# Optimization experiments

Measured on AMD Instinct MI355X. Metric: run time of the kernel, lower is better.

The kernel has to match this reference:

```python
import jax, jax.numpy as jnp
import numpy as np

COORD_DIM = 2
NUM_CHANNELS = 3
LATENT = 128
HIDDEN = 64
N0 = 8192
RADIUS = 0.035
RADII = (RADIUS, 2.0 * RADIUS)
ITER_COUNT = 3


def _radius_edges(y, x, r):
    # y: (Ny,d) source points, x: (Nx,d) query points -> edge lists (src into y, dst into x)
    d2 = ((x[:, None, :] - y[None, :, :]) ** 2).sum(-1)
    dst, src = np.nonzero(d2 <= r * r)
    return jnp.asarray(src, jnp.int32), jnp.asarray(dst, jnp.int32)


def setup_inputs():
    rng = np.random.default_rng(0)
    coords_np = rng.uniform(size=(COORD_DIM, N0)).astype(np.float32)
    c0 = coords_np.T            # (N0, d) fine level
    c1 = coords_np[:, ::2].T    # (N1, d) coarse level (stride-2 subsample)
    r_cross = max(RADII)
    e01_src, e01_dst = _radius_edges(c0, c1, r_cross)   # GK_0_1: y=lvl0, x=lvl1
    e10_src, e10_dst = _radius_edges(c1, c0, r_cross)   # GK_1_0: y=lvl1, x=lvl0
    e00_src, e00_dst = _radius_edges(c0, c0, RADII[0])  # GK_0_0
    e11_src, e11_dst = _radius_edges(c1, c1, RADII[1])  # GK_1_1

    key = jax.random.key(0)
    ks = iter(jax.random.split(key, 40))

    def lin(fi, fo):
        return jax.random.normal(next(ks), (fi, fo), jnp.float32) / np.float32(np.sqrt(fi))

    inp = dict(
        coords=jnp.asarray(coords_np),
        samples=jax.random.normal(next(ks), (N0, NUM_CHANNELS), jnp.float32),
        sigma=jax.random.uniform(next(ks), (1,), jnp.float32),
        fc_lift_w=lin(NUM_CHANNELS, LATENT), fc_lift_b=jnp.zeros((LATENT,), jnp.float32),
        fc_proj_w=lin(LATENT, NUM_CHANNELS), fc_proj_b=jnp.zeros((NUM_CHANNELS,), jnp.float32),
        W0_w=lin(LATENT, LATENT), W0_b=jnp.zeros((LATENT,), jnp.float32),
        W1_w=lin(LATENT, LATENT), W1_b=jnp.zeros((LATENT,), jnp.float32),
    )
    for name in ("gk00", "gk01", "gk10", "gk11"):
        inp[name + "_w1"] = lin(2 * COORD_DIM, HIDDEN)
        inp[name + "_b1"] = jnp.zeros((HIDDEN,), jnp.float32)
        inp[name + "_w2"] = lin(HIDDEN, LATENT)
        inp[name + "_b2"] = jnp.zeros((LATENT,), jnp.float32)
    inp.update(e00_src=e00_src, e00_dst=e00_dst, e01_src=e01_src, e01_dst=e01_dst,
               e10_src=e10_src, e10_dst=e10_dst, e11_src=e11_src, e11_dst=e11_dst)
    return inp


def _gno(xc, yc, f_y, src, dst, w1, b1, w2, b2, num_x):
    # gather -> edge kernel MLP on concat coords -> modulate by f_y -> scatter-mean
    e = jnp.concatenate([yc[src], xc[dst]], axis=1)        # (E, 2d)
    k = jax.nn.gelu(e @ w1 + b1) @ w2 + b2                 # (E, C) kernel values
    msg = k * f_y[src]                                     # 'linear' integral transform
    out = jax.ops.segment_sum(msg, dst, num_segments=num_x)
    cnt = jax.ops.segment_sum(jnp.ones(src.shape, msg.dtype), dst, num_segments=num_x)
    return out / jnp.maximum(cnt, 1.0)[:, None]


def reference(coords, samples, sigma,
              fc_lift_w, fc_lift_b, fc_proj_w, fc_proj_b,
              W0_w, W0_b, W1_w, W1_b,
              gk00_w1, gk00_b1, gk00_w2, gk00_b2,
              gk01_w1, gk01_b1, gk01_w2, gk01_b2,
              gk10_w1, gk10_b1, gk10_w2, gk10_b2,
              gk11_w1, gk11_b1, gk11_w2, gk11_b2,
              e00_src, e00_dst, e01_src, e01_dst,
              e10_src, e10_dst, e11_src, e11_dst):
    c0 = coords.T            # (N0, d)
    c1 = coords[:, ::2].T    # (N1, d)
    n0, n1 = c0.shape[0], c1.shape[0]
    v_down0 = samples @ fc_lift_w + fc_lift_b   # lifted features, never overwritten at level 0
    v_up0 = v_down0
    v_up1 = None
    for _ in range(ITER_COUNT):
        # downward pass (l = 1)
        vd = _gno(c1, c0, v_down0, e01_src, e01_dst, gk01_w1, gk01_b1, gk01_w2, gk01_b2, n1)
        if v_up1 is not None:
            vd = vd + v_up1
        v_down1 = jax.nn.relu(vd)
        # bottom level update
        v_up1 = jax.nn.relu(v_down1 @ W1_w + W1_b
                            + _gno(c1, c1, v_down1, e11_src, e11_dst, gk11_w1, gk11_b1, gk11_w2, gk11_b2, n1))
        # upward pass (l = 0)
        vu = _gno(c0, c1, v_up1, e10_src, e10_dst, gk10_w1, gk10_b1, gk10_w2, gk10_b2, n0)
        vu = vu + v_down0 @ W0_w + W0_b \
             + _gno(c0, c0, v_down0, e00_src, e00_dst, gk00_w1, gk00_b1, gk00_w2, gk00_b2, n0)
        v_up0 = jax.nn.relu(vu)
    return v_up0 @ fc_proj_w + fc_proj_b   # (N0, num_channels)
```

## Files before the change

### kernel.cpp

```cpp
#include <hip/hip_runtime.h>
#include <hip/hip_bf16.h>

typedef __attribute__((ext_vector_type(8))) short s8;
typedef __attribute__((ext_vector_type(4))) float f4;

__device__ __forceinline__ float gelu_fast(float x) {
    float x2 = x * x;
    float k  = x * fmaf(x2, 0.07135481624f, 1.59576912161f);
    float e  = __expf(k);
    float r  = __builtin_amdgcn_rcpf(e + 1.f);
    return x - x * r;
}

__device__ __forceinline__ short f2bf_bits(float v) {
    __hip_bfloat16 b = __float2bfloat16(v);
    return *(short*)&b;
}

struct RP { const int* edst; int E; int N; int* rowptr; };

__global__ void rowptr4_kernel(RP a, RP b, RP c, RP d) {
    RP g = (blockIdx.y == 0) ? a : (blockIdx.y == 1) ? b : (blockIdx.y == 2) ? c : d;
    int i = blockIdx.x * blockDim.x + threadIdx.x;
    if (i >= g.E) return;
    int dd = g.edst[i];
    int p  = (i == 0) ? -1 : g.edst[i - 1];
    for (int r = p + 1; r <= dd; ++r) g.rowptr[r] = i;
    if (i == g.E - 1)
        for (int r = dd + 1; r <= g.N; ++r) g.rowptr[r] = g.E;
}

__global__ __launch_bounds__(128) void pack_w2_kernel(
    const float* __restrict__ wa, const float* __restrict__ wb,
    const float* __restrict__ wc, const float* __restrict__ wd,
    short* __restrict__ out)
{
    const float* w2 = (blockIdx.x == 0) ? wa : (blockIdx.x == 1) ? wb
                    : (blockIdx.x == 2) ? wc : wd;
    short* dst = out + (size_t)blockIdx.x * 8192;
    const int t = threadIdx.x;
    const int w = t >> 6, lane = t & 63, q = (lane >> 4), n = lane & 15;
#pragma unroll
    for (int T = 0; T < 4; ++T)
#pragma unroll
        for (int s = 0; s < 2; ++s)
#pragma unroll
            for (int j = 0; j < 8; ++j) {
                int k  = s * 32 + q * 8 + j;
                int ch = 64 * w + 16 * T + n;
                dst[((((w * 4 + T) * 2 + s) * 64) + lane) * 8 + j] =
                    f2bf_bits(w2[k * 128 + ch]);
            }
}

__global__ __launch_bounds__(128) void gno_kernel(
    const float* __restrict__ coords, int n0, int sx, int sy,
    const float* __restrict__ f_y,
    const int* __restrict__ esrc, const int* __restrict__ rowptr,
    const float* __restrict__ w1, const float* __restrict__ b1,
    const short* __restrict__ w2bf, const float* __restrict__ b2,
    const float* __restrict__ add0, const float* __restrict__ add1,
    int do_relu, float* __restrict__ out,
    const float* __restrict__ projw, const float* __restrict__ projb,
    float* __restrict__ fout)
{
    const int b = blockIdx.x, t = threadIdx.x;
    const int w = t >> 6, lane = t & 63, q = lane >> 4, n = lane & 15;
    const int h = lane;

    __shared__ int   s_src[16];
    __shared__ float s_yx[16], s_yy[16];
    __shared__ __align__(16) short s_gb[16 * 72];
    __shared__ float sred[6];

    const float rw0 = w1[h], rw1 = w1[64 + h];
    const float xcx = coords[(long)b * sx];
    const float xcy = coords[n0 + (long)b * sx];
    const float xcc = xcx * w1[128 + h] + xcy * w1[192 + h] + b1[h];

    s8 bfrag[4][2];
    const s8* w2f = (const s8*)w2bf;
#pragma unroll
    for (int T = 0; T < 4; ++T)
#pragma unroll
        for (int s = 0; s < 2; ++s)
            bfrag[T][s] = w2f[((w * 4 + T) * 2 + s) * 64 + lane];

    float b2c[4];
#pragma unroll
    for (int T = 0; T < 4; ++T) b2c[T] = b2[w * 64 + T * 16 + n];

    const int lo = rowptr[b], hi = rowptr[b + 1];

    float acc4[4] = {0.f, 0.f, 0.f, 0.f};

    for (int base = lo; base < hi; base += 16) {
        const int cnt = min(16, hi - base);
        if (t < 16) {
            int e = base + t; if (e >= hi) e = hi - 1;
            int sv = esrc[e];
            s_src[t] = sv;
            s_yx[t]  = coords[(long)sv * sy];
            s_yy[t]  = coords[n0 + (long)sv * sy];
        }
        __syncthreads();
        float fv[4][4];
#pragma unroll
        for (int r = 0; r < 4; ++r) {
            int m = q * 4 + r;
            bool valid = m < cnt;
            long srow = (long)s_src[m] * 128;
#pragma unroll
            for (int T = 0; T < 4; ++T)
                fv[r][T] = valid ? f_y[srow + w * 64 + T * 16 + n] : 0.f;
        }
#pragma unroll
        for (int i = 0; i < 8; ++i) {
            int j = 2 * i + w;
            float x = fmaf(s_yx[j], rw0, fmaf(s_yy[j], rw1, xcc));
            s_gb[j * 72 + h] = f2bf_bits(gelu_fast(x));
        }
        __syncthreads();
        const s8 a0 = *(const s8*)&s_gb[n * 72 + q * 8];
        const s8 a1 = *(const s8*)&s_gb[n * 72 + q * 8 + 32];
        f4 c[4];
#pragma unroll
        for (int T = 0; T < 4; ++T) {
            f4 z = {0.f, 0.f, 0.f, 0.f};
            z = __builtin_amdgcn_mfma_f32_16x16x32_bf16(a0, bfrag[T][0], z, 0, 0, 0);
            c[T] = __builtin_amdgcn_mfma_f32_16x16x32_bf16(a1, bfrag[T][1], z, 0, 0, 0);
        }
#pragma unroll
        for (int r = 0; r < 4; ++r)
#pragma unroll
            for (int T = 0; T < 4; ++T)
                acc4[T] += (c[T][r] + b2c[T]) * fv[r][T];
    }

    const float inv = 1.f / fmaxf((float)(hi - lo), 1.f);
    float res4[4];
#pragma unroll
    for (int T = 0; T < 4; ++T) {
        float v = acc4[T];
        v += __shfl_xor(v, 16, 64);
        v += __shfl_xor(v, 32, 64);
        long o = (long)b * 128 + w * 64 + T * 16 + n;
        float res = v * inv;
        if (add0) res += add0[o];
        if (add1) res += add1[o];
        if (do_relu) res = fmaxf(res, 0.f);
        res4[T] = res;
    }
    if (!projw) {
        if (q == 0)
#pragma unroll
            for (int T = 0; T < 4; ++T)
                out[(long)b * 128 + w * 64 + T * 16 + n] = res4[T];
    } else {
        __syncthreads();
        float* s_pr = (float*)s_gb;
        if (q == 0)
#pragma unroll
            for (int T = 0; T < 4; ++T) s_pr[w * 64 + T * 16 + n] = res4[T];
        __syncthreads();
        float v = s_pr[t];
        float p0 = v * projw[t * 3 + 0];
        float p1 = v * projw[t * 3 + 1];
        float p2 = v * projw[t * 3 + 2];
#pragma unroll
        for (int o = 32; o > 0; o >>= 1) {
            p0 += __shfl_down(p0, o);
            p1 += __shfl_down(p1, o);
            p2 += __shfl_down(p2, o);
        }
        if (lane == 0) { sred[w * 3 + 0] = p0; sred[w * 3 + 1] = p1; sred[w * 3 + 2] = p2; }
        __syncthreads();
        if (t < 3) fout[b * 3 + t] = sred[t] + sred[3 + t] + projb[t];
    }
}

__global__ __launch_bounds__(128) void fused_relu_mm_kernel(
    const float* __restrict__ base, const float* __restrict__ addl,
    float* __restrict__ vout,
    const float* __restrict__ W, const float* __restrict__ bias,
    float* __restrict__ out, int R)
{
    const int r0 = blockIdx.x * 8;
    const int t = threadIdx.x;
    __shared__ float s_x[8 * 128];
#pragma unroll
    for (int j = 0; j < 8; ++j) {
        int r = r0 + j;
        if (r < R) {
            long o = (long)r * 128 + t;
            float v = base[o] + (addl ? addl[o] : 0.f);
            v = fmaxf(v, 0.f);
            s_x[j * 128 + t] = v;
            vout[o] = v;
        } else s_x[j * 128 + t] = 0.f;
    }
    __syncthreads();
    float acc[8];
    const float bc = bias[t];
#pragma unroll
    for (int j = 0; j < 8; ++j) acc[j] = bc;
    for (int hh = 0; hh < 128; ++hh) {
        float wv = W[hh * 128 + t];
#pragma unroll
        for (int j = 0; j < 8; ++j) acc[j] += s_x[j * 128 + hh] * wv;
    }
#pragma unroll
    for (int j = 0; j < 8; ++j) {
        int r = r0 + j;
        if (r < R) out[(long)r * 128 + t] = acc[j];
    }
}

__global__ __launch_bounds__(128) void matmul128_kernel(
    const float* __restrict__ X, const float* __restrict__ W,
    const float* __restrict__ bias, float* __restrict__ out, int R)
{
    const int r0 = blockIdx.x * 8;
    const int t = threadIdx.x;
    __shared__ float s_x[8 * 128];
#pragma unroll
    for (int j = 0; j < 8; ++j) {
        int r = r0 + j;
        s_x[j * 128 + t] = (r < R) ? X[(long)r * 128 + t] : 0.f;
    }
    __syncthreads();
    float acc[8];
    const float bc = bias[t];
#pragma unroll
    for (int j = 0; j < 8; ++j) acc[j] = bc;
    for (int hh = 0; hh < 128; ++hh) {
        float wv = W[hh * 128 + t];
#pragma unroll
        for (int j = 0; j < 8; ++j) acc[j] += s_x[j * 128 + hh] * wv;
    }
#pragma unroll
    for (int j = 0; j < 8; ++j) {
        int r = r0 + j;
        if (r < R) out[(long)r * 128 + t] = acc[j];
    }
}

__global__ __launch_bounds__(128) void lift_kernel(
    const float* __restrict__ samples, const float* __restrict__ W,
    const float* __restrict__ bias, float* __restrict__ out, int N)
{
    const int i = blockIdx.x;
    const int t = threadIdx.x;
    float s0 = samples[i * 3 + 0];
    float s1 = samples[i * 3 + 1];
    float s2 = samples[i * 3 + 2];
    out[(long)i * 128 + t] = s0 * W[t] + s1 * W[128 + t] + s2 * W[256 + t] + bias[t];
}

extern "C" void kernel_launch(void* const* d_in, const int* in_sizes, int n_in,
                              void* d_out, int out_size, void* d_ws, size_t ws_size,
                              hipStream_t stream)
{
    const float* coords  = (const float*)d_in[0];
    const float* samples = (const float*)d_in[1];
    const float* lift_w  = (const float*)d_in[3];
    const float* lift_b  = (const float*)d_in[4];
    const float* proj_w  = (const float*)d_in[5];
    const float* proj_b  = (const float*)d_in[6];
    const float* W0_w    = (const float*)d_in[7];
    const float* W0_b    = (const float*)d_in[8];
    const float* W1_w    = (const float*)d_in[9];
    const float* W1_b    = (const float*)d_in[10];
    const float *gw1[4], *gb1[4], *gw2[4], *gb2[4];
    for (int g = 0; g < 4; ++g) {
        gw1[g] = (const float*)d_in[11 + 4 * g + 0];
        gb1[g] = (const float*)d_in[11 + 4 * g + 1];
        gw2[g] = (const float*)d_in[11 + 4 * g + 2];
        gb2[g] = (const float*)d_in[11 + 4 * g + 3];
    }
    const int* es[4]; const int* ed[4]; int E[4];
    for (int g = 0; g < 4; ++g) {
        es[g] = (const int*)d_in[27 + 2 * g];
        ed[g] = (const int*)d_in[27 + 2 * g + 1];
        E[g]  = in_sizes[27 + 2 * g];
    }

    const int N0 = in_sizes[0] / 2;
    const int N1 = (N0 + 1) / 2;

    float* ws = (float*)d_ws;
    float* v_down0 = ws;
    float* w0term  = v_down0 + (size_t)N0 * 128;
    float* gno00o  = w0term  + (size_t)N0 * 128;
    float* gno01b  = gno00o  + (size_t)N0 * 128;
    float* v_down1 = gno01b  + (size_t)N1 * 128;
    float* w1term  = v_down1 + (size_t)N1 * 128;
    float* v_up1   = w1term  + (size_t)N1 * 128;
    short* w2pack  = (short*)(v_up1 + (size_t)N1 * 128);
    int*   rp      = (int*)(w2pack + 4 * 8192);
    int* rp00 = rp;
    int* rp01 = rp00 + (N0 + 1);
    int* rp10 = rp01 + (N1 + 1);
    int* rp11 = rp10 + (N0 + 1);
    int* rptr[4] = {rp00, rp01, rp10, rp11};
    int  rpN[4]  = {N0, N1, N0, N1};

    {
        int maxE = E[0];
        for (int g = 1; g < 4; ++g) maxE = max(maxE, E[g]);
        RP a = {ed[0], E[0], rpN[0], rptr[0]};
        RP b = {ed[1], E[1], rpN[1], rptr[1]};
        RP c = {ed[2], E[2], rpN[2], rptr[2]};
        RP d = {ed[3], E[3], rpN[3], rptr[3]};
        dim3 grid((maxE + 255) / 256, 4);
        rowptr4_kernel<<<grid, 256, 0, stream>>>(a, b, c, d);
    }
    pack_w2_kernel<<<4, 128, 0, stream>>>(gw2[0], gw2[1], gw2[2], gw2[3], w2pack);

    lift_kernel<<<N0, 128, 0, stream>>>(samples, lift_w, lift_b, v_down0, N0);
    matmul128_kernel<<<(N0 + 7) / 8, 128, 0, stream>>>(v_down0, W0_w, W0_b, w0term, N0);
    gno_kernel<<<N0, 128, 0, stream>>>(coords, N0, 1, 1, v_down0,
        es[0], rp00, gw1[0], gb1[0], w2pack + 0 * 8192, gb2[0],
        nullptr, nullptr, 0, gno00o, nullptr, nullptr, nullptr);
    gno_kernel<<<N1, 128, 0, stream>>>(coords, N0, 2, 1, v_down0,
        es[1], rp01, gw1[1], gb1[1], w2pack + 1 * 8192, gb2[1],
        nullptr, nullptr, 0, gno01b, nullptr, nullptr, nullptr);

    for (int it = 0; it < 3; ++it) {
        fused_relu_mm_kernel<<<(N1 + 7) / 8, 128, 0, stream>>>(
            gno01b, (it == 0) ? nullptr : v_up1, v_down1, W1_w, W1_b, w1term, N1);
        gno_kernel<<<N1, 128, 0, stream>>>(coords, N0, 2, 2, v_down1,
            es[3], rp11, gw1[3], gb1[3], w2pack + 3 * 8192, gb2[3],
            w1term, nullptr, 1, v_up1, nullptr, nullptr, nullptr);
    }

    gno_kernel<<<N0, 128, 0, stream>>>(coords, N0, 1, 2, v_up1,
        es[2], rp10, gw1[2], gb1[2], w2pack + 2 * 8192, gb2[2],
        w0term, gno00o, 1, nullptr, proj_w, proj_b, (float*)d_out);
}
```

Measured before the change: 368.5 us.

## Process multiple destination nodes per GNO block with double-buffered edge staging

Each GNO block now handles a chunk of consecutive destination nodes (4 at fine level, 2 at coarse) so it can reuse the loaded W2 fragments and layer-1 weights. Edge source indices and coordinates are prefetched 64 at a time into double-buffered shared memory, and the GELU tile buffer is also double-buffered so one barrier per 16-edge group can be dropped. W2 is repacked so each lane owns four contiguous output channels, which turns feature gathers, bias and output stores into float4 accesses. The grid shrinks, so there are fewer blocks to hide latency, and the loop control becomes more complex.

```diff
diff --git a/kernel.cpp b/kernel.cpp
--- a/kernel.cpp
+++ b/kernel.cpp
@@ -47,7 +47,7 @@
 #pragma unroll
             for (int j = 0; j < 8; ++j) {
                 int k  = s * 32 + q * 8 + j;
-                int ch = 64 * w + 16 * T + n;
+                int ch = 64 * w + 4 * n + T;
                 dst[((((w * 4 + T) * 2 + s) * 64) + lane) * 8 + j] =
                     f2bf_bits(w2[k * 128 + ch]);
             }
@@ -57,6 +57,7 @@
     const float* __restrict__ coords, int n0, int sx, int sy,
     const float* __restrict__ f_y,
     const int* __restrict__ esrc, const int* __restrict__ rowptr,
+    int N, int chunk,
     const float* __restrict__ w1, const float* __restrict__ b1,
     const short* __restrict__ w2bf, const float* __restrict__ b2,
     const float* __restrict__ add0, const float* __restrict__ add1,
@@ -64,20 +65,23 @@
     const float* __restrict__ projw, const float* __restrict__ projb,
     float* __restrict__ fout)
 {
-    const int b = blockIdx.x, t = threadIdx.x;
+    const int t = threadIdx.x;
     const int w = t >> 6, lane = t & 63, q = lane >> 4, n = lane & 15;
-    const int h = lane;
-
-    __shared__ int   s_src[16];
-    __shared__ float s_yx[16], s_yy[16];
-    __shared__ __align__(16) short s_gb[16 * 72];
+    const int d0 = blockIdx.x * chunk;
+    if (d0 >= N) return;
+    const int d1 = min(d0 + chunk, N);
+
+    __shared__ int   s_rp[8];
+    __shared__ int   s_src[2][64];
+    __shared__ float s_yx[2][64], s_yy[2][64];
+    __shared__ __align__(16) short s_gb[2][16 * 72];
+    __shared__ float s_pr[128];
     __shared__ float sred[6];
 
-    const float rw0 = w1[h], rw1 = w1[64 + h];
-    const float xcx = coords[(long)b * sx];
-    const float xcy = coords[n0 + (long)b * sx];
-    const float xcc = xcx * w1[128 + h] + xcy * w1[192 + h] + b1[h];
-
+    if (t <= d1 - d0) s_rp[t] = rowptr[d0 + t];
+
+    const float rw0 = w1[lane], rw1 = w1[64 + lane];
+    const float rwx = w1[128 + lane], rwy = w1[192 + lane], rb1 = b1[lane];
     s8 bfrag[4][2];
     const s8* w2f = (const s8*)w2bf;
 #pragma unroll
@@ -85,97 +89,148 @@
 #pragma unroll
         for (int s = 0; s < 2; ++s)
             bfrag[T][s] = w2f[((w * 4 + T) * 2 + s) * 64 + lane];
-
-    float b2c[4];
-#pragma unroll
-    for (int T = 0; T < 4; ++T) b2c[T] = b2[w * 64 + T * 16 + n];
-
-    const int lo = rowptr[b], hi = rowptr[b + 1];
-
-    float acc4[4] = {0.f, 0.f, 0.f, 0.f};
-
-    for (int base = lo; base < hi; base += 16) {
-        const int cnt = min(16, hi - base);
-        if (t < 16) {
-            int e = base + t; if (e >= hi) e = hi - 1;
-            int sv = esrc[e];
-            s_src[t] = sv;
-            s_yx[t]  = coords[(long)sv * sy];
-            s_yy[t]  = coords[n0 + (long)sv * sy];
+    const f4 b2c = *(const f4*)&b2[w * 64 + 4 * n];
+
+    __syncthreads();
+
+    int sd, sbase = 0, shi = 0;
+    {
+        int i = 0;
+        while (d0 + i < d1 && s_rp[i] == s_rp[i + 1]) ++i;
+        sd = d0 + i;
+        if (sd < d1) { sbase = s_rp[i]; shi = s_rp[i + 1]; }
+    }
+    int cb = 0;
+    if (sd < d1 && t < 64) {
+        int e = sbase + t; if (e >= shi) e = shi - 1;
+        int sv = esrc[e];
+        s_src[0][t] = sv;
+        s_yx[0][t]  = coords[(long)sv * sy];
+        s_yy[0][t]  = coords[n0 + (long)sv * sy];
+    }
+    __syncthreads();
+
+    int gbp = 0;
+    float cxx = coords[(long)d0 * sx];
+    float cxy = coords[n0 + (long)d0 * sx];
+
+    for (int d = d0; d < d1; ++d) {
+        float nxx = 0.f, nxy = 0.f;
+        if (d + 1 < d1) {
+            nxx = coords[(long)(d + 1) * sx];
+            nxy = coords[n0 + (long)(d + 1) * sx];
         }
-        __syncthreads();
-        float fv[4][4];
-#pragma unroll
-        for (int r = 0; r < 4; ++r) {
-            int m = q * 4 + r;
-            bool valid = m < cnt;
-            long srow = (long)s_src[m] * 128;
-#pragma unroll
-            for (int T = 0; T < 4; ++T)
-                fv[r][T] = valid ? f_y[srow + w * 64 + T * 16 + n] : 0.f;
+        const int lo = s_rp[d - d0], hi = s_rp[d - d0 + 1];
+        const float xcc = fmaf(cxx, rwx, fmaf(cxy, rwy, rb1));
+        f4 acc = {0.f, 0.f, 0.f, 0.f};
+
+        for (int ss = lo; ss < hi; ss += 64) {
+            {
+                int nsd = sd, nsbase = sbase + 64, nshi = shi;
+                if (nsbase >= nshi) {
+                    int i = nsd - d0 + 1;
+                    while (d0 + i < d1 && s_rp[i] == s_rp[i + 1]) ++i;
+                    nsd = d0 + i;
+                    if (nsd < d1) { nsbase = s_rp[i]; nshi = s_rp[i + 1]; }
+                }
+                if (nsd < d1 && t < 64) {
+                    int e = nsbase + t; if (e >= nshi) e = nshi - 1;
+                    int sv = esrc[e];
+                    s_src[cb ^ 1][t] = sv;
+                    s_yx[cb ^ 1][t]  = coords[(long)sv * sy];
+                    s_yy[cb ^ 1][t]  = coords[n0 + (long)sv * sy];
+                }
+                sd = nsd; sbase = nsbase; shi = nshi;
+            }
+            const int ssn = min(64, hi - ss);
+            for (int goff = 0; goff < ssn; goff += 16) {
+                const int cnt = min(16, ssn - goff);
+                f4 fv[4];
+#pragma unroll
+                for (int r = 0; r < 4; ++r) {
+                    int m = q * 4 + r;
+                    if (m < cnt) {
+                        long srow = (long)s_src[cb][goff + m] * 128;
+                        fv[r] = *(const f4*)&f_y[srow + w * 64 + 4 * n];
+                    } else {
+                        f4 z = {0.f, 0.f, 0.f, 0.f};
+                        fv[r] = z;
+                    }
+                }
+#pragma unroll
+                for (int i = 0; i < 8; ++i) {
+                    int j = 2 * i + w;
+                    int p = goff + j;
+                    float x = fmaf(s_yx[cb][p], rw0, fmaf(s_yy[cb][p], rw1, xcc));
+                    s_gb[gbp][j * 72 + lane] = f2bf_bits(gelu_fast(x));
+                }
+                __syncthreads();
+                const s8 a0 = *(const s8*)&s_gb[gbp][n * 72 + q * 8];
+                const s8 a1 = *(const s8*)&s_gb[gbp][n * 72 + q * 8 + 32];
+                f4 c[4];
+#pragma unroll
+                for (int T = 0; T < 4; ++T) {
+                    f4 z = {0.f, 0.f, 0.f, 0.f};
+                    z = __builtin_amdgcn_mfma_f32_16x16x32_bf16(a0, bfrag[T][0], z, 0, 0, 0);
+                    c[T] = __builtin_amdgcn_mfma_f32_16x16x32_bf16(a1, bfrag[T][1], z, 0, 0, 0);
+                }
+#pragma unroll
+                for (int r = 0; r < 4; ++r)
+#pragma unroll
+                    for (int T = 0; T < 4; ++T)
+                        acc[T] += (c[T][r] + b2c[T]) * fv[r][T];
+                gbp ^= 1;
+            }
+            cb ^= 1;
         }
-#pragma unroll
-        for (int i = 0; i < 8; ++i) {
-            int j = 2 * i + w;
-            float x = fmaf(s_yx[j], rw0, fmaf(s_yy[j], rw1, xcc));
-            s_gb[j * 72 + h] = f2bf_bits(gelu_fast(x));
+
+        const float inv = 1.f / fmaxf((float)(hi - lo), 1.f);
+        f4 res;
+#pragma unroll
+        for (int T = 0; T < 4; ++T) {
+            float v = acc[T];
+            v += __shfl_xor(v, 16, 64);
+            v += __shfl_xor(v, 32, 64);
+            res[T] = v * inv;
         }
-        __syncthreads();
-        const s8 a0 = *(const s8*)&s_gb[n * 72 + q * 8];
-        const s8 a1 = *(const s8*)&s_gb[n * 72 + q * 8 + 32];
-        f4 c[4];
-#pragma unroll
-        for (int T = 0; T < 4; ++T) {
-            f4 z = {0.f, 0.f, 0.f, 0.f};
-            z = __builtin_amdgcn_mfma_f32_16x16x32_bf16(a0, bfrag[T][0], z, 0, 0, 0);
-            c[T] = __builtin_amdgcn_mfma_f32_16x16x32_bf16(a1, bfrag[T][1], z, 0, 0, 0);
+        const long obase = (long)d * 128 + w * 64 + 4 * n;
+        if (!projw) {
+            if (q == 0) {
+                if (add0) res += *(const f4*)&add0[obase];
+                if (add1) res += *(const f4*)&add1[obase];
+                if (do_relu) {
+#pragma unroll
+                    for (int T = 0; T < 4; ++T) res[T] = fmaxf(res[T], 0.f);
+                }
+                *(f4*)&out[obase] = res;
+            }
+        } else {
+            __syncthreads();
+            if (q == 0) {
+                if (add0) res += *(const f4*)&add0[obase];
+                if (add1) res += *(const f4*)&add1[obase];
+                if (do_relu) {
+#pragma unroll
+                    for (int T = 0; T < 4; ++T) res[T] = fmaxf(res[T], 0.f);
+                }
+                *(f4*)&s_pr[w * 64 + 4 * n] = res;
+            }
+            __syncthreads();
+            float v = s_pr[t];
+            float p0 = v * projw[t * 3 + 0];
+            float p1 = v * projw[t * 3 + 1];
+            float p2 = v * projw[t * 3 + 2];
+#pragma unroll
+            for (int o = 32; o > 0; o >>= 1) {
+                p0 += __shfl_down(p0, o);
+                p1 += __shfl_down(p1, o);
+                p2 += __shfl_down(p2, o);
+            }
+            if (lane == 0) { sred[w * 3 + 0] = p0; sred[w * 3 + 1] = p1; sred[w * 3 + 2] = p2; }
+            __syncthreads();
+            if (t < 3) fout[d * 3 + t] = sred[t] + sred[3 + t] + projb[t];
         }
-#pragma unroll
-        for (int r = 0; r < 4; ++r)
-#pragma unroll
-            for (int T = 0; T < 4; ++T)
-                acc4[T] += (c[T][r] + b2c[T]) * fv[r][T];
-    }
-
-    const float inv = 1.f / fmaxf((float)(hi - lo), 1.f);
-    float res4[4];
-#pragma unroll
-    for (int T = 0; T < 4; ++T) {
-        float v = acc4[T];
-        v += __shfl_xor(v, 16, 64);
-        v += __shfl_xor(v, 32, 64);
-        long o = (long)b * 128 + w * 64 + T * 16 + n;
-        float res = v * inv;
-        if (add0) res += add0[o];
-        if (add1) res += add1[o];
-        if (do_relu) res = fmaxf(res, 0.f);
-        res4[T] = res;
-    }
-    if (!projw) {
-        if (q == 0)
-#pragma unroll
-            for (int T = 0; T < 4; ++T)
-                out[(long)b * 128 + w * 64 + T * 16 + n] = res4[T];
-    } else {
-        __syncthreads();
-        float* s_pr = (float*)s_gb;
-        if (q == 0)
-#pragma unroll
-            for (int T = 0; T < 4; ++T) s_pr[w * 64 + T * 16 + n] = res4[T];
-        __syncthreads();
-        float v = s_pr[t];
-        float p0 = v * projw[t * 3 + 0];
-        float p1 = v * projw[t * 3 + 1];
-        float p2 = v * projw[t * 3 + 2];
-#pragma unroll
-        for (int o = 32; o > 0; o >>= 1) {
-            p0 += __shfl_down(p0, o);
-            p1 += __shfl_down(p1, o);
-            p2 += __shfl_down(p2, o);
-        }
-        if (lane == 0) { sred[w * 3 + 0] = p0; sred[w * 3 + 1] = p1; sred[w * 3 + 2] = p2; }
-        __syncthreads();
-        if (t < 3) fout[b * 3 + t] = sred[t] + sred[3 + t] + projb[t];
+        cxx = nxx; cxy = nxy;
     }
 }
 
@@ -302,16 +357,14 @@
     int* rp01 = rp00 + (N0 + 1);
     int* rp10 = rp01 + (N1 + 1);
     int* rp11 = rp10 + (N0 + 1);
-    int* rptr[4] = {rp00, rp01, rp10, rp11};
-    int  rpN[4]  = {N0, N1, N0, N1};
 
     {
         int maxE = E[0];
         for (int g = 1; g < 4; ++g) maxE = max(maxE, E[g]);
-        RP a = {ed[0], E[0], rpN[0], rptr[0]};
-        RP b = {ed[1], E[1], rpN[1], rptr[1]};
-        RP c = {ed[2], E[2], rpN[2], rptr[2]};
-        RP d = {ed[3], E[3], rpN[3], rptr[3]};
+        RP a = {ed[0], E[0], N0, rp00};
+        RP b = {ed[1], E[1], N1, rp01};
+        RP c = {ed[2], E[2], N0, rp10};
+        RP d = {ed[3], E[3], N1, rp11};
         dim3 grid((maxE + 255) / 256, 4);
         rowptr4_kernel<<<grid, 256, 0, stream>>>(a, b, c, d);
     }
@@ -319,22 +372,24 @@
 
     lift_kernel<<<N0, 128, 0, stream>>>(samples, lift_w, lift_b, v_down0, N0);
     matmul128_kernel<<<(N0 + 7) / 8, 128, 0, stream>>>(v_down0, W0_w, W0_b, w0term, N0);
-    gno_kernel<<<N0, 128, 0, stream>>>(coords, N0, 1, 1, v_down0,
-        es[0], rp00, gw1[0], gb1[0], w2pack + 0 * 8192, gb2[0],
+
+    const int CH0 = 4, CH1 = 2;
+    gno_kernel<<<(N0 + CH0 - 1) / CH0, 128, 0, stream>>>(coords, N0, 1, 1, v_down0,
+        es[0], rp00, N0, CH0, gw1[0], gb1[0], w2pack + 0 * 8192, gb2[0],
         nullptr, nullptr, 0, gno00o, nullptr, nullptr, nullptr);
-    gno_kernel<<<N1, 128, 0, stream>>>(coords, N0, 2, 1, v_down0,
-        es[1], rp01, gw1[1], gb1[1], w2pack + 1 * 8192, gb2[1],
+    gno_kernel<<<(N1 + CH1 - 1) / CH1, 128, 0, stream>>>(coords, N0, 2, 1, v_down0,
+        es[1], rp01, N1, CH1, gw1[1], gb1[1], w2pack + 1 * 8192, gb2[1],
         nullptr, nullptr, 0, gno01b, nullptr, nullptr, nullptr);
 
     for (int it = 0; it < 3; ++it) {
         fused_relu_mm_kernel<<<(N1 + 7) / 8, 128, 0, stream>>>(
             gno01b, (it == 0) ? nullptr : v_up1, v_down1, W1_w, W1_b, w1term, N1);
-        gno_kernel<<<N1, 128, 0, stream>>>(coords, N0, 2, 2, v_down1,
-            es[3], rp11, gw1[3], gb1[3], w2pack + 3 * 8192, gb2[3],
+        gno_kernel<<<(N1 + CH1 - 1) / CH1, 128, 0, stream>>>(coords, N0, 2, 2, v_down1,
+            es[3], rp11, N1, CH1, gw1[3], gb1[3], w2pack + 3 * 8192, gb2[3],
             w1term, nullptr, 1, v_up1, nullptr, nullptr, nullptr);
     }
 
-    gno_kernel<<<N0, 128, 0, stream>>>(coords, N0, 1, 2, v_up1,
-        es[2], rp10, gw1[2], gb1[2], w2pack + 2 * 8192, gb2[2],
+    gno_kernel<<<(N0 + CH0 - 1) / CH0, 128, 0, stream>>>(coords, N0, 1, 2, v_up1,
+        es[2], rp10, N0, CH0, gw1[2], gb1[2], w2pack + 2 * 8192, gb2[2],
         w0term, gno00o, 1, nullptr, proj_w, proj_b, (float*)d_out);
 }
```

Result: slower. 454.5 us (+23.3%).

## Switch GNO to edge-tiled blocks with atomic segment accumulation and separate epilogue

Applied to the files above, without the earlier changes.

Replaces the one-block-per-destination-node GNO kernel with a kernel that processes fixed tiles of 64 edges, finds destination segment boundaries with a ballot, and atomically adds per-segment partial sums into a zeroed accumulator. Mean normalization, residual adds, ReLU and final projection move to separate epilogue kernels. The W2 packing is changed so each lane gets four contiguous channels, which allows vectorized f4 loads of source features. This is meant to fix load imbalance from uneven node degrees and raise utilization of blocks with few edges. In exchange it adds zeroing and epilogue launches, global atomics, and extra memory traffic.

```diff
diff --git a/kernel.cpp b/kernel.cpp
--- a/kernel.cpp
+++ b/kernel.cpp
@@ -3,6 +3,8 @@
 
 typedef __attribute__((ext_vector_type(8))) short s8;
 typedef __attribute__((ext_vector_type(4))) float f4;
+
+#define TILE 64
 
 __device__ __forceinline__ float gelu_fast(float x) {
     float x2 = x * x;
@@ -47,37 +49,46 @@
 #pragma unroll
             for (int j = 0; j < 8; ++j) {
                 int k  = s * 32 + q * 8 + j;
-                int ch = 64 * w + 16 * T + n;
+                int ch = 64 * w + 4 * n + T;
                 dst[((((w * 4 + T) * 2 + s) * 64) + lane) * 8 + j] =
                     f2bf_bits(w2[k * 128 + ch]);
             }
 }
 
-__global__ __launch_bounds__(128) void gno_kernel(
+__global__ __launch_bounds__(128) void gno_edge_kernel(
     const float* __restrict__ coords, int n0, int sx, int sy,
     const float* __restrict__ f_y,
-    const int* __restrict__ esrc, const int* __restrict__ rowptr,
+    const int* __restrict__ esrc, const int* __restrict__ edst, int E,
     const float* __restrict__ w1, const float* __restrict__ b1,
     const short* __restrict__ w2bf, const float* __restrict__ b2,
-    const float* __restrict__ add0, const float* __restrict__ add1,
-    int do_relu, float* __restrict__ out,
-    const float* __restrict__ projw, const float* __restrict__ projb,
-    float* __restrict__ fout)
-{
-    const int b = blockIdx.x, t = threadIdx.x;
+    float* __restrict__ acc)
+{
+    const int t = threadIdx.x;
     const int w = t >> 6, lane = t & 63, q = lane >> 4, n = lane & 15;
-    const int h = lane;
-
-    __shared__ int   s_src[16];
-    __shared__ float s_yx[16], s_yy[16];
-    __shared__ __align__(16) short s_gb[16 * 72];
-    __shared__ float sred[6];
-
-    const float rw0 = w1[h], rw1 = w1[64 + h];
-    const float xcx = coords[(long)b * sx];
-    const float xcy = coords[n0 + (long)b * sx];
-    const float xcc = xcx * w1[128 + h] + xcy * w1[192 + h] + b1[h];
-
+    const int e0 = blockIdx.x * TILE;
+    const int te = min(TILE, E - e0);
+
+    __shared__ int   s_src[TILE], s_dst[TILE];
+    __shared__ float s_yx[TILE], s_yy[TILE], s_xx[TILE], s_xy[TILE];
+    __shared__ __align__(16) short s_gb[2][16 * 72];
+
+    if (t < TILE) {
+        int e = min(e0 + t, E - 1);
+        int sv = esrc[e];
+        s_src[t] = sv;
+        s_yx[t]  = coords[(long)sv * sy];
+        s_yy[t]  = coords[n0 + (long)sv * sy];
+    } else {
+        int l = t - TILE;
+        int e = min(e0 + l, E - 1);
+        int dv = edst[e];
+        s_dst[l] = dv;
+        s_xx[l]  = coords[(long)dv * sx];
+        s_xy[l]  = coords[n0 + (long)dv * sx];
+    }
+
+    const float rw0 = w1[lane], rw1v = w1[64 + lane];
+    const float rwx = w1[128 + lane], rwy = w1[192 + lane], rb1 = b1[lane];
     s8 bfrag[4][2];
     const s8* w2f = (const s8*)w2bf;
 #pragma unroll
@@ -85,98 +96,114 @@
 #pragma unroll
         for (int s = 0; s < 2; ++s)
             bfrag[T][s] = w2f[((w * 4 + T) * 2 + s) * 64 + lane];
-
-    float b2c[4];
-#pragma unroll
-    for (int T = 0; T < 4; ++T) b2c[T] = b2[w * 64 + T * 16 + n];
-
-    const int lo = rowptr[b], hi = rowptr[b + 1];
-
-    float acc4[4] = {0.f, 0.f, 0.f, 0.f};
-
-    for (int base = lo; base < hi; base += 16) {
-        const int cnt = min(16, hi - base);
-        if (t < 16) {
-            int e = base + t; if (e >= hi) e = hi - 1;
-            int sv = esrc[e];
-            s_src[t] = sv;
-            s_yx[t]  = coords[(long)sv * sy];
-            s_yy[t]  = coords[n0 + (long)sv * sy];
+    const f4 b2c = *(const f4*)&b2[w * 64 + 4 * n];
+
+    __syncthreads();
+
+    bool fl = (lane < te) && (lane == te - 1 || s_dst[lane + 1] != s_dst[lane]);
+    unsigned long long segmask = __ballot(fl);
+
+    int gbp = 0;
+    int a = 0;
+    while (a < te) {
+        const int b = a + 1 + (int)__builtin_ctzll(segmask >> a);
+        const int dcur = s_dst[a];
+        f4 accr = {0.f, 0.f, 0.f, 0.f};
+
+        for (int g0 = a; g0 < b; g0 += 16) {
+            const int cnt = min(16, b - g0);
+            f4 fv[4];
+#pragma unroll
+            for (int r = 0; r < 4; ++r) {
+                int m = q * 4 + r;
+                if (m < cnt) {
+                    long srow = (long)s_src[g0 + m] * 128;
+                    fv[r] = *(const f4*)&f_y[srow + w * 64 + 4 * n];
+                } else {
+                    f4 z = {0.f, 0.f, 0.f, 0.f};
+                    fv[r] = z;
+                }
+            }
+#pragma unroll
+            for (int i = 0; i < 8; ++i) {
+                int j = 2 * i + w;
+                int p = min(g0 + j, te - 1);
+                float x = fmaf(s_yx[p], rw0, fmaf(s_yy[p], rw1v,
+                          fmaf(s_xx[p], rwx, fmaf(s_xy[p], rwy, rb1))));
+                s_gb[gbp][j * 72 + lane] = f2bf_bits(gelu_fast(x));
+            }
+            __syncthreads();
+            const s8 a0 = *(const s8*)&s_gb[gbp][n * 72 + q * 8];
+            const s8 a1 = *(const s8*)&s_gb[gbp][n * 72 + q * 8 + 32];
+            f4 c[4];
+#pragma unroll
+            for (int T = 0; T < 4; ++T) {
+                f4 z = {0.f, 0.f, 0.f, 0.f};
+                z = __builtin_amdgcn_mfma_f32_16x16x32_bf16(a0, bfrag[T][0], z, 0, 0, 0);
+                c[T] = __builtin_amdgcn_mfma_f32_16x16x32_bf16(a1, bfrag[T][1], z, 0, 0, 0);
+            }
+#pragma unroll
+            for (int r = 0; r < 4; ++r)
+#pragma unroll
+                for (int T = 0; T < 4; ++T)
+                    accr[T] += (c[T][r] + b2c[T]) * fv[r][T];
+            gbp ^= 1;
         }
-        __syncthreads();
-        float fv[4][4];
-#pragma unroll
-        for (int r = 0; r < 4; ++r) {
-            int m = q * 4 + r;
-            bool valid = m < cnt;
-            long srow = (long)s_src[m] * 128;
-#pragma unroll
-            for (int T = 0; T < 4; ++T)
-                fv[r][T] = valid ? f_y[srow + w * 64 + T * 16 + n] : 0.f;
+
+#pragma unroll
+        for (int T = 0; T < 4; ++T) {
+            float v = accr[T];
+            v += __shfl_xor(v, 16, 64);
+            v += __shfl_xor(v, 32, 64);
+            if (q == 0)
+                atomicAdd(&acc[(long)dcur * 128 + w * 64 + 4 * n + T], v);
         }
-#pragma unroll
-        for (int i = 0; i < 8; ++i) {
-            int j = 2 * i + w;
-            float x = fmaf(s_yx[j], rw0, fmaf(s_yy[j], rw1, xcc));
-            s_gb[j * 72 + h] = f2bf_bits(gelu_fast(x));
-        }
-        __syncthreads();
-        const s8 a0 = *(const s8*)&s_gb[n * 72 + q * 8];
-        const s8 a1 = *(const s8*)&s_gb[n * 72 + q * 8 + 32];
-        f4 c[4];
-#pragma unroll
-        for (int T = 0; T < 4; ++T) {
-            f4 z = {0.f, 0.f, 0.f, 0.f};
-            z = __builtin_amdgcn_mfma_f32_16x16x32_bf16(a0, bfrag[T][0], z, 0, 0, 0);
-            c[T] = __builtin_amdgcn_mfma_f32_16x16x32_bf16(a1, bfrag[T][1], z, 0, 0, 0);
-        }
-#pragma unroll
-        for (int r = 0; r < 4; ++r)
-#pragma unroll
-            for (int T = 0; T < 4; ++T)
-                acc4[T] += (c[T][r] + b2c[T]) * fv[r][T];
-    }
-
-    const float inv = 1.f / fmaxf((float)(hi - lo), 1.f);
-    float res4[4];
-#pragma unroll
-    for (int T = 0; T < 4; ++T) {
-        float v = acc4[T];
-        v += __shfl_xor(v, 16, 64);
-        v += __shfl_xor(v, 32, 64);
-        long o = (long)b * 128 + w * 64 + T * 16 + n;
-        float res = v * inv;
-        if (add0) res += add0[o];
-        if (add1) res += add1[o];
-        if (do_relu) res = fmaxf(res, 0.f);
-        res4[T] = res;
-    }
-    if (!projw) {
-        if (q == 0)
-#pragma unroll
-            for (int T = 0; T < 4; ++T)
-                out[(long)b * 128 + w * 64 + T * 16 + n] = res4[T];
-    } else {
-        __syncthreads();
-        float* s_pr = (float*)s_gb;
-        if (q == 0)
-#pragma unroll
-            for (int T = 0; T < 4; ++T) s_pr[w * 64 + T * 16 + n] = res4[T];
-        __syncthreads();
-        float v = s_pr[t];
-        float p0 = v * projw[t * 3 + 0];
-        float p1 = v * projw[t * 3 + 1];
-        float p2 = v * projw[t * 3 + 2];
-#pragma unroll
-        for (int o = 32; o > 0; o >>= 1) {
-            p0 += __shfl_down(p0, o);
-            p1 += __shfl_down(p1, o);
-            p2 += __shfl_down(p2, o);
-        }
-        if (lane == 0) { sred[w * 3 + 0] = p0; sred[w * 3 + 1] = p1; sred[w * 3 + 2] = p2; }
-        __syncthreads();
-        if (t < 3) fout[b * 3 + t] = sred[t] + sred[3 + t] + projb[t];
-    }
+        a = b;
+    }
+}
+
+__global__ void zero_kernel(float* __restrict__ p, long n) {
+    long i = ((long)blockIdx.x * 256 + threadIdx.x) * 4;
+    if (i < n) { f4 z = {0.f, 0.f, 0.f, 0.f}; *(f4*)&p[i] = z; }
+}
+
+__global__ __launch_bounds__(256) void epi_kernel(
+    float* __restrict__ acc, const int* __restrict__ rowptr,
+    const float* __restrict__ add0, int do_relu, int N)
+{
+    long idx = (long)blockIdx.x * 256 + threadIdx.x;
+    if (idx >= (long)N * 128) return;
+    int d = idx >> 7;
+    float deg = (float)(rowptr[d + 1] - rowptr[d]);
+    float res = acc[idx] / fmaxf(deg, 1.f);
+    if (add0) res += add0[idx];
+    if (do_relu) res = fmaxf(res, 0.f);
+    acc[idx] = res;
+}
+
+__global__ __launch_bounds__(128) void epi_proj_kernel(
+    const float* __restrict__ acc, const int* __restrict__ rowptr,
+    const float* __restrict__ add0, const float* __restrict__ add1,
+    const float* __restrict__ projw, const float* __restrict__ projb,
+    float* __restrict__ fout, int N)
+{
+    const int d = blockIdx.x, t = threadIdx.x;
+    float deg = (float)(rowptr[d + 1] - rowptr[d]);
+    long o = (long)d * 128 + t;
+    float res = fmaxf(acc[o] / fmaxf(deg, 1.f) + add0[o] + add1[o], 0.f);
+    float p0 = res * projw[t * 3 + 0];
+    float p1 = res * projw[t * 3 + 1];
+    float p2 = res * projw[t * 3 + 2];
+#pragma unroll
+    for (int off = 32; off > 0; off >>= 1) {
+        p0 += __shfl_down(p0, off);
+        p1 += __shfl_down(p1, off);
+        p2 += __shfl_down(p2, off);
+    }
+    __shared__ float sred[6];
+    if ((t & 63) == 0) { int w = t >> 6; sred[w * 3 + 0] = p0; sred[w * 3 + 1] = p1; sred[w * 3 + 2] = p2; }
+    __syncthreads();
+    if (t < 3) fout[d * 3 + t] = sred[t] + sred[3 + t] + projb[t];
 }
 
 __global__ __launch_bounds__(128) void fused_relu_mm_kernel(
@@ -302,16 +329,14 @@
     int* rp01 = rp00 + (N0 + 1);
     int* rp10 = rp01 + (N1 + 1);
     int* rp11 = rp10 + (N0 + 1);
-    int* rptr[4] = {rp00, rp01, rp10, rp11};
-    int  rpN[4]  = {N0, N1, N0, N1};
 
     {
         int maxE = E[0];
         for (int g = 1; g < 4; ++g) maxE = max(maxE, E[g]);
-        RP a = {ed[0], E[0], rpN[0], rptr[0]};
-        RP b = {ed[1], E[1], rpN[1], rptr[1]};
-        RP c = {ed[2], E[2], rpN[2], rptr[2]};
-        RP d = {ed[3], E[3], rpN[3], rptr[3]};
+        RP a = {ed[0], E[0], N0, rp00};
+        RP b = {ed[1], E[1], N1, rp01};
+        RP c = {ed[2], E[2], N0, rp10};
+        RP d = {ed[3], E[3], N1, rp11};
         dim3 grid((maxE + 255) / 256, 4);
         rowptr4_kernel<<<grid, 256, 0, stream>>>(a, b, c, d);
     }
@@ -319,22 +344,29 @@
 
     lift_kernel<<<N0, 128, 0, stream>>>(samples, lift_w, lift_b, v_down0, N0);
     matmul128_kernel<<<(N0 + 7) / 8, 128, 0, stream>>>(v_down0, W0_w, W0_b, w0term, N0);
-    gno_kernel<<<N0, 128, 0, stream>>>(coords, N0, 1, 1, v_down0,
-        es[0], rp00, gw1[0], gb1[0], w2pack + 0 * 8192, gb2[0],
-        nullptr, nullptr, 0, gno00o, nullptr, nullptr, nullptr);
-    gno_kernel<<<N1, 128, 0, stream>>>(coords, N0, 2, 1, v_down0,
-        es[1], rp01, gw1[1], gb1[1], w2pack + 1 * 8192, gb2[1],
-        nullptr, nullptr, 0, gno01b, nullptr, nullptr, nullptr);
+
+    const long n00 = (long)N0 * 128, n11 = (long)N1 * 128;
+
+    zero_kernel<<<(int)((n00 + n11) / 4 + 255) / 256, 256, 0, stream>>>(gno00o, n00 + n11);
+    gno_edge_kernel<<<(E[0] + TILE - 1) / TILE, 128, 0, stream>>>(coords, N0, 1, 1,
+        v_down0, es[0], ed[0], E[0], gw1[0], gb1[0], w2pack + 0 * 8192, gb2[0], gno00o);
+    gno_edge_kernel<<<(E[1] + TILE - 1) / TILE, 128, 0, stream>>>(coords, N0, 2, 1,
+        v_down0, es[1], ed[1], E[1], gw1[1], gb1[1], w2pack + 1 * 8192, gb2[1], gno01b);
+    epi_kernel<<<(int)(n00 + 255) / 256, 256, 0, stream>>>(gno00o, rp00, nullptr, 0, N0);
+    epi_kernel<<<(int)(n11 + 255) / 256, 256, 0, stream>>>(gno01b, rp01, nullptr, 0, N1);
 
     for (int it = 0; it < 3; ++it) {
         fused_relu_mm_kernel<<<(N1 + 7) / 8, 128, 0, stream>>>(
             gno01b, (it == 0) ? nullptr : v_up1, v_down1, W1_w, W1_b, w1term, N1);
-        gno_kernel<<<N1, 128, 0, stream>>>(coords, N0, 2, 2, v_down1,
-            es[3], rp11, gw1[3], gb1[3], w2pack + 3 * 8192, gb2[3],
-            w1term, nullptr, 1, v_up1, nullptr, nullptr, nullptr);
-    }
-
-    gno_kernel<<<N0, 128, 0, stream>>>(coords, N0, 1, 2, v_up1,
-        es[2], rp10, gw1[2], gb1[2], w2pack + 2 * 8192, gb2[2],
-        w0term, gno00o, 1, nullptr, proj_w, proj_b, (float*)d_out);
-}
+        zero_kernel<<<(int)(n11 / 4 + 255) / 256, 256, 0, stream>>>(v_up1, n11);
+        gno_edge_kernel<<<(E[3] + TILE - 1) / TILE, 128, 0, stream>>>(coords, N0, 2, 2,
+            v_down1, es[3], ed[3], E[3], gw1[3], gb1[3], w2pack + 3 * 8192, gb2[3], v_up1);
+        epi_kernel<<<(int)(n11 + 255) / 256, 256, 0, stream>>>(v_up1, rp11, w1term, 1, N1);
+    }
+
+    zero_kernel<<<(int)(n00 / 4 + 255) / 256, 256, 0, stream>>>(v_down0, n00);
+    gno_edge_kernel<<<(E[2] + TILE - 1) / TILE, 128, 0, stream>>>(coords, N0, 1, 2,
+        v_up1, es[2], ed[2], E[2], gw1[2], gb1[2], w2pack + 2 * 8192, gb2[2], v_down0);
+    epi_proj_kernel<<<N0, 128, 0, stream>>>(v_down0, rp10, w0term, gno00o,
+        proj_w, proj_b, (float*)d_out, N0);
+}
```

After: 442.8 us. +20.2%, slower.
